# Kernel optimization log

Hardware: AMD Instinct MI355X
Metric: run time of the kernel (lower is better)

## Reference

```python
import jax, jax.numpy as jnp
import numpy as np

IOU_THRESHOLD = 0.3
NUM_CLASSES = 80
BG_IDX = NUM_CLASSES
EPS = 1e-09
TOPK_FALLBACK = 3


def _make_boxes(key, shape, img=640.0):
    # shape = (..., 4); produce valid x1y1x2y2 boxes
    k1, k2 = jax.random.split(key)
    xy = jax.random.uniform(k1, shape[:-1] + (2,)) * img
    wh = jax.random.uniform(k2, shape[:-1] + (2,)) * 128.0 + 8.0
    return jnp.concatenate([xy - wh / 2, xy + wh / 2], axis=-1).astype(jnp.float32)


def setup_inputs() -> dict:
    key = jax.random.key(0)
    ks = jax.random.split(key, 6)
    bs, A, G = 16, 33600, 64
    pd_scores = jax.random.normal(ks[0], (bs, A, NUM_CLASSES), dtype=jnp.float32)
    pd_bboxes = _make_boxes(ks[1], (bs, A, 4))
    anc_points = jax.random.uniform(ks[2], (A, 2), dtype=jnp.float32) * 640.0
    gt_labels = jax.random.randint(ks[3], (bs, G, 1), 0, NUM_CLASSES).astype(jnp.int64)
    gt_bboxes = _make_boxes(ks[4], (bs, G, 4))
    mask_gt = jax.random.randint(ks[5], (bs, G, 1), 0, 2).astype(jnp.int32)
    return {"pd_scores": pd_scores, "pd_bboxes": pd_bboxes, "anc_points": anc_points,
            "gt_labels": gt_labels, "gt_bboxes": gt_bboxes, "mask_gt": mask_gt}


def _pairwise_iou(gt, pd):
    # gt: (bs, G, 4), pd: (bs, A, 4) -> (bs, G, A)
    b1 = gt[:, :, None, :]   # (bs, G, 1, 4)
    b2 = pd[:, None, :, :]   # (bs, 1, A, 4)
    iw = jnp.clip(jnp.minimum(b1[..., 2], b2[..., 2]) - jnp.maximum(b1[..., 0], b2[..., 0]), 0)
    ih = jnp.clip(jnp.minimum(b1[..., 3], b2[..., 3]) - jnp.maximum(b1[..., 1], b2[..., 1]), 0)
    inter = iw * ih
    a1 = (b1[..., 2] - b1[..., 0]) * (b1[..., 3] - b1[..., 1])
    a2 = (b2[..., 2] - b2[..., 0]) * (b2[..., 3] - b2[..., 1])
    return inter / (a1 + a2 - inter + EPS)


def reference(pd_scores, pd_bboxes, anc_points, gt_labels, gt_bboxes, mask_gt):
    bs, G, _ = gt_bboxes.shape
    A = anc_points.shape[0]
    valid = mask_gt[..., 0].astype(bool)                      # (bs, G)

    # IoU matrix; rows of invalid GTs are zero (original writes only valid rows)
    overlaps = _pairwise_iou(gt_bboxes, pd_bboxes) * valid[:, :, None]  # (bs, G, A)

    pos_mask = (overlaps > IOU_THRESHOLD) & valid[:, :, None]
    fg_any = pos_mask.any(axis=(1, 2))                        # (bs,)

    # Per-batch top-k fallback when a batch has zero positives but has valid GTs
    masked = jnp.where(valid[:, :, None], overlaps, -jnp.inf)
    top_vals, _ = jax.lax.top_k(masked.reshape(bs, G * A), TOPK_FALLBACK)
    min_iou = top_vals[:, -1]                                 # (bs,)
    fb_pos = (overlaps >= min_iou[:, None, None]) & valid[:, :, None]
    has_valid = valid.any(axis=1)
    need_fb = (~fg_any) & has_valid
    pos_mask = jnp.where(need_fb[:, None, None], fb_pos, pos_mask)
    fg_mask = pos_mask.any(axis=1)                            # (bs, A)

    # Assignment: argmax over GT axis (first-max, like torch.argmax)
    target_gt_idx = jnp.argmax(overlaps, axis=1)              # (bs, A)

    batch_idx = jnp.arange(bs)[:, None]
    valid_assign = valid[batch_idx, target_gt_idx]            # (bs, A)
    mask = fg_mask & valid_assign

    labels_g = gt_labels[..., 0][batch_idx, target_gt_idx]    # (bs, A)
    target_labels = jnp.where(mask, labels_g, BG_IDX).astype(jnp.int64)
    boxes_g = gt_bboxes[batch_idx, target_gt_idx]             # (bs, A, 4)
    target_bboxes = boxes_g * mask[..., None].astype(boxes_g.dtype)
    # one_hot zeroes out-of-range class indices, matching the explicit range check
    target_scores = jax.nn.one_hot(labels_g, NUM_CLASSES, dtype=jnp.float32) * mask[..., None]

    return (target_labels, target_bboxes, target_scores, fg_mask, target_gt_idx)
```

## Files before the change

### kernel.cpp

```cpp
#include <hip/hip_runtime.h>
#include <math.h>

#define NC 80
constexpr int BS  = 16;
constexpr int NA  = 33600;
constexpr int NG  = 64;
constexpr int TPB = 256;
constexpr int NBLK = (NA + TPB - 1) / TPB;
constexpr int NW   = TPB / 64;
constexpr int NC4  = NC / 4;

typedef float f32x4 __attribute__((ext_vector_type(4)));

__device__ __forceinline__ void ins3(float v, float& t0, float& t1, float& t2) {
  t2 = fmaxf(t2, fminf(v, t1));
  t1 = fmaxf(t1, fminf(v, t0));
  t0 = fmaxf(t0, v);
}

__device__ __forceinline__ void wave_top3(float& t0, float& t1, float& t2) {
  #pragma unroll
  for (int off = 32; off > 0; off >>= 1) {
    float u0 = __shfl_xor(t0, off, 64);
    float u1 = __shfl_xor(t1, off, 64);
    float u2 = __shfl_xor(t2, off, 64);
    ins3(u0, t0, t1, t2);
    ins3(u1, t0, t1, t2);
    ins3(u2, t0, t1, t2);
  }
}

__global__ __launch_bounds__(TPB) void p1_kernel(
    const float4* __restrict__ pd, const float4* __restrict__ gt,
    const int* __restrict__ glab, const int* __restrict__ gmask,
    float* __restrict__ outL, float4* __restrict__ outB,
    float* __restrict__ outS, float* __restrict__ outF,
    float* __restrict__ outI, float* __restrict__ blockTop)
{
  #pragma clang fp contract(off)
  const int b   = blockIdx.y;
  const int tid = threadIdx.x;

  __shared__ float4 sbox[NG];
  __shared__ float  sarea[NG];
  __shared__ int    slab[NG];
  __shared__ int    svalid[NG];
  __shared__ int    scls[TPB];

  const int a0  = blockIdx.x * TPB;
  const int a   = a0 + tid;
  const bool inb = a < NA;

  float4 p = make_float4(0.f, 0.f, 0.f, 0.f);
  if (inb) p = pd[(long)b * NA + a];

  if (tid < NG) {
    int v = gmask[b * NG + tid];
    float4 g = gt[b * NG + tid];
    if (!v) g = make_float4(0.f, 0.f, 0.f, 0.f);
    sbox[tid]   = g;
    sarea[tid]  = (g.z - g.x) * (g.w - g.y);
    slab[tid]   = glab[b * NG + tid];
    svalid[tid] = v;
  }
  __syncthreads();

  float best = -1.f;
  int   bidx = 0;
  float a2 = 0.f;
  bool  maskv = false;
  int   blab  = 0;

  if (inb) {
    a2 = (p.z - p.x) * (p.w - p.y);
    #pragma unroll 8
    for (int g = 0; g < NG; ++g) {
      float4 gb = sbox[g];
      float iw = fminf(gb.z, p.z) - fmaxf(gb.x, p.x);
      float ih = fminf(gb.w, p.w) - fmaxf(gb.y, p.y);
      iw = fmaxf(iw, 0.f);
      ih = fmaxf(ih, 0.f);
      float inter = iw * ih;
      float den   = sarea[g] + a2 - inter + 1e-9f;
      float iou   = inter / den;
      bidx = (iou > best) ? g : bidx;
      best = fmaxf(best, iou);
    }
    bool fg = best > 0.3f;
    maskv = fg && (svalid[bidx] != 0);
    blab  = slab[bidx];
    long ga = (long)b * NA + a;
    outL[ga] = maskv ? (float)blab : 80.f;
    float m = maskv ? 1.f : 0.f;
    float4 gb = sbox[bidx];
    outB[ga] = make_float4(gb.x * m, gb.y * m, gb.z * m, gb.w * m);
    outF[ga] = fg ? 1.f : 0.f;
    outI[ga] = (float)bidx;
  }
  scls[tid] = maskv ? blab : -1;

  float wmax = best;
  #pragma unroll
  for (int off = 32; off > 0; off >>= 1)
    wmax = fmaxf(wmax, __shfl_xor(wmax, off, 64));

  float* bt = blockTop + (((long)b * NBLK + blockIdx.x) * NW + (tid >> 6)) * 3;

  if (wmax <= 0.3f) {
    float t0 = -INFINITY, t1 = -INFINITY, t2 = -INFINITY;
    if (inb) {
      #pragma unroll 4
      for (int g = 0; g < NG; ++g) {
        float4 gb = sbox[g];
        float iw = fminf(gb.z, p.z) - fmaxf(gb.x, p.x);
        float ih = fminf(gb.w, p.w) - fmaxf(gb.y, p.y);
        iw = fmaxf(iw, 0.f);
        ih = fmaxf(ih, 0.f);
        float inter = iw * ih;
        float den   = sarea[g] + a2 - inter + 1e-9f;
        float iou   = inter / den;
        ins3(iou, t0, t1, t2);
      }
    }
    wave_top3(t0, t1, t2);
    if ((tid & 63) == 0) { bt[1] = t1; bt[2] = t2; }
  }
  if ((tid & 63) == 0) bt[0] = wmax;

  __syncthreads();

  const int nA   = min(TPB, NA - a0);
  const int cnt4 = nA * NC4;
  f32x4* s4 = reinterpret_cast<f32x4*>(outS + ((long)b * NA + a0) * NC);
  for (int i = tid; i < cnt4; i += TPB) {
    int row = i / NC4;
    int c0  = (i - row * NC4) * 4;
    int cls = scls[row];
    f32x4 v;
    v.x = (cls == c0    ) ? 1.f : 0.f;
    v.y = (cls == c0 + 1) ? 1.f : 0.f;
    v.z = (cls == c0 + 2) ? 1.f : 0.f;
    v.w = (cls == c0 + 3) ? 1.f : 0.f;
    __builtin_nontemporal_store(v, s4 + i);
  }
}

__global__ __launch_bounds__(TPB) void p3_kernel(
    const float4* __restrict__ pd, const float4* __restrict__ gt,
    const int* __restrict__ glab, const int* __restrict__ gmask,
    const float* __restrict__ blockTop,
    float* __restrict__ outL, float4* __restrict__ outB,
    float* __restrict__ outS, float* __restrict__ outF)
{
  #pragma clang fp contract(off)
  const int b   = blockIdx.y;
  const int tid = threadIdx.x;

  __shared__ float  swm[NW];
  __shared__ float  sM;
  __shared__ float  swt[NW][3];
  __shared__ float  sres;
  __shared__ int    sfb;
  __shared__ float4 sbox[NG];
  __shared__ float  sarea[NG];
  __shared__ int    slab[NG];
  __shared__ int    svalid[NG];

  float m = -INFINITY;
  for (int i = tid; i < NBLK * NW; i += TPB)
    m = fmaxf(m, blockTop[((long)b * NBLK * NW + i) * 3]);
  #pragma unroll
  for (int off = 32; off > 0; off >>= 1)
    m = fmaxf(m, __shfl_xor(m, off, 64));
  const int lane = tid & 63, wid = tid >> 6;
  if (lane == 0) swm[wid] = m;
  __syncthreads();
  if (tid == 0) {
    float r = swm[0];
    #pragma unroll
    for (int w = 1; w < NW; ++w) r = fmaxf(r, swm[w]);
    sM = r;
  }
  __syncthreads();
  if (sM > 0.3f) return;

  int gv = (tid < NG) ? gmask[b * NG + tid] : 0;
  unsigned long long bal = __ballot(gv != 0);

  float t0 = -INFINITY, t1 = -INFINITY, t2 = -INFINITY;
  for (int i = tid; i < NBLK * NW; i += TPB) {
    const float* bt = blockTop + ((long)b * NBLK * NW + i) * 3;
    ins3(bt[0], t0, t1, t2);
    ins3(bt[1], t0, t1, t2);
    ins3(bt[2], t0, t1, t2);
  }
  wave_top3(t0, t1, t2);
  if (lane == 0) { swt[wid][0] = t0; swt[wid][1] = t1; swt[wid][2] = t2; }
  __syncthreads();
  if (tid == 0) {
    float r0 = swt[0][0], r1 = swt[0][1], r2 = swt[0][2];
    #pragma unroll
    for (int w = 1; w < NW; ++w) {
      ins3(swt[w][0], r0, r1, r2);
      ins3(swt[w][1], r0, r1, r2);
      ins3(swt[w][2], r0, r1, r2);
    }
    sfb  = (!(r0 > 0.3f) && bal != 0ULL) ? 1 : 0;
    sres = r2;
  }
  if (tid < NG) {
    float4 g = gt[b * NG + tid];
    if (!gv) g = make_float4(0.f, 0.f, 0.f, 0.f);
    sbox[tid]   = g;
    sarea[tid]  = (g.z - g.x) * (g.w - g.y);
    slab[tid]   = glab[b * NG + tid];
    svalid[tid] = gv;
  }
  __syncthreads();
  if (sfb == 0) return;
  const float minio = sres;

  const int a = blockIdx.x * TPB + tid;
  if (a >= NA) return;

  float4 p  = pd[(long)b * NA + a];
  float  a2 = (p.z - p.x) * (p.w - p.y);
  float best = -1.f;
  int   bidx = 0;
  #pragma unroll 8
  for (int g = 0; g < NG; ++g) {
    float4 gb = sbox[g];
    float iw = fminf(gb.z, p.z) - fmaxf(gb.x, p.x);
    float ih = fminf(gb.w, p.w) - fmaxf(gb.y, p.y);
    iw = fmaxf(iw, 0.f);
    ih = fmaxf(ih, 0.f);
    float inter = iw * ih;
    float den   = sarea[g] + a2 - inter + 1e-9f;
    float iou   = inter / den;
    bidx = (iou > best) ? g : bidx;
    best = fmaxf(best, iou);
  }
  bool fg    = best >= minio;
  bool maskv = fg && (svalid[bidx] != 0);
  int  blab  = slab[bidx];
  long ga = (long)b * NA + a;
  outL[ga] = maskv ? (float)blab : 80.f;
  float mm = maskv ? 1.f : 0.f;
  float4 gb = sbox[bidx];
  outB[ga] = make_float4(gb.x * mm, gb.y * mm, gb.z * mm, gb.w * mm);
  outF[ga] = fg ? 1.f : 0.f;
  if (maskv) outS[ga * NC + blab] = 1.f;
}

extern "C" void kernel_launch(void* const* d_in, const int* in_sizes, int n_in,
                              void* d_out, int out_size, void* d_ws, size_t ws_size,
                              hipStream_t stream) {
  const float4* pd    = (const float4*)d_in[1];
  const int*    glab  = (const int*)d_in[3];
  const float4* gt    = (const float4*)d_in[4];
  const int*    gmask = (const int*)d_in[5];

  float* outf = (float*)d_out;
  float*  outL = outf;
  float4* outB = (float4*)(outf + (long)BS * NA);
  float*  outS = outf + (long)BS * NA * 5;
  float*  outF = outf + (long)BS * NA * 5 + (long)BS * NA * NC;
  float*  outI = outF + (long)BS * NA;

  float* blockTop = (float*)d_ws;

  dim3 grid(NBLK, BS);
  p1_kernel<<<grid, TPB, 0, stream>>>(pd, gt, glab, gmask,
                                      outL, outB, outS, outF, outI, blockTop);
  p3_kernel<<<grid, TPB, 0, stream>>>(pd, gt, glab, gmask, blockTop,
                                      outL, outB, outS, outF);
}
```

Measured before the change: 284.6 us.

## Write one-hot scores per wave via shuffles and shrink fallback grid to one block per batch

In p1, each wave now writes the one-hot score rows for its own 64 anchors, taking class indices from lanes with shuffles instead of a shared array. This removes the block-wide barrier and the shared-memory staging before the large store loop. p3 now launches one block per batch, and that block loops over all anchors. Previously every one of the many blocks re-reduced the whole blockTop array only to exit early. The cost is that the fallback path, when it is taken, runs serially on only 16 blocks, which would be very slow for that case.

Result: no change. 282.2 us (-0.9%).

```diff
diff --git a/kernel.cpp b/kernel.cpp
--- a/kernel.cpp
+++ b/kernel.cpp
@@ -45,7 +45,6 @@
   __shared__ float  sarea[NG];
   __shared__ int    slab[NG];
   __shared__ int    svalid[NG];
-  __shared__ int    scls[TPB];
 
   const int a0  = blockIdx.x * TPB;
   const int a   = a0 + tid;
@@ -97,14 +96,34 @@
     outF[ga] = fg ? 1.f : 0.f;
     outI[ga] = (float)bidx;
   }
-  scls[tid] = maskv ? blab : -1;
+
+  const int lane = tid & 63, wid = tid >> 6;
+  const int nA    = min(TPB, NA - a0);
+  const int wrow0 = wid * 64;
+  const int rows  = min(64, nA - wrow0);
+  const int own_cls = maskv ? blab : -1;
+  if (rows > 0) {
+    f32x4* s4 = reinterpret_cast<f32x4*>(outS + ((long)b * NA + a0 + wrow0) * NC);
+    const int cnt4 = rows * NC4;
+    for (int i = lane; i < cnt4; i += 64) {
+      int row = i / NC4;
+      int c0  = (i - row * NC4) * 4;
+      int cls = __shfl(own_cls, row, 64);
+      f32x4 v;
+      v.x = (cls == c0    ) ? 1.f : 0.f;
+      v.y = (cls == c0 + 1) ? 1.f : 0.f;
+      v.z = (cls == c0 + 2) ? 1.f : 0.f;
+      v.w = (cls == c0 + 3) ? 1.f : 0.f;
+      __builtin_nontemporal_store(v, s4 + i);
+    }
+  }
 
   float wmax = best;
   #pragma unroll
   for (int off = 32; off > 0; off >>= 1)
     wmax = fmaxf(wmax, __shfl_xor(wmax, off, 64));
 
-  float* bt = blockTop + (((long)b * NBLK + blockIdx.x) * NW + (tid >> 6)) * 3;
+  float* bt = blockTop + (((long)b * NBLK + blockIdx.x) * NW + wid) * 3;
 
   if (wmax <= 0.3f) {
     float t0 = -INFINITY, t1 = -INFINITY, t2 = -INFINITY;
@@ -123,26 +142,9 @@
       }
     }
     wave_top3(t0, t1, t2);
-    if ((tid & 63) == 0) { bt[1] = t1; bt[2] = t2; }
-  }
-  if ((tid & 63) == 0) bt[0] = wmax;
-
-  __syncthreads();
-
-  const int nA   = min(TPB, NA - a0);
-  const int cnt4 = nA * NC4;
-  f32x4* s4 = reinterpret_cast<f32x4*>(outS + ((long)b * NA + a0) * NC);
-  for (int i = tid; i < cnt4; i += TPB) {
-    int row = i / NC4;
-    int c0  = (i - row * NC4) * 4;
-    int cls = scls[row];
-    f32x4 v;
-    v.x = (cls == c0    ) ? 1.f : 0.f;
-    v.y = (cls == c0 + 1) ? 1.f : 0.f;
-    v.z = (cls == c0 + 2) ? 1.f : 0.f;
-    v.w = (cls == c0 + 3) ? 1.f : 0.f;
-    __builtin_nontemporal_store(v, s4 + i);
-  }
+    if (lane == 0) { bt[1] = t1; bt[2] = t2; }
+  }
+  if (lane == 0) bt[0] = wmax;
 }
 
 __global__ __launch_bounds__(TPB) void p3_kernel(
@@ -153,7 +155,7 @@
     float* __restrict__ outS, float* __restrict__ outF)
 {
   #pragma clang fp contract(off)
-  const int b   = blockIdx.y;
+  const int b   = blockIdx.x;
   const int tid = threadIdx.x;
 
   __shared__ float  swm[NW];
@@ -220,36 +222,35 @@
   if (sfb == 0) return;
   const float minio = sres;
 
-  const int a = blockIdx.x * TPB + tid;
-  if (a >= NA) return;
-
-  float4 p  = pd[(long)b * NA + a];
-  float  a2 = (p.z - p.x) * (p.w - p.y);
-  float best = -1.f;
-  int   bidx = 0;
-  #pragma unroll 8
-  for (int g = 0; g < NG; ++g) {
-    float4 gb = sbox[g];
-    float iw = fminf(gb.z, p.z) - fmaxf(gb.x, p.x);
-    float ih = fminf(gb.w, p.w) - fmaxf(gb.y, p.y);
-    iw = fmaxf(iw, 0.f);
-    ih = fmaxf(ih, 0.f);
-    float inter = iw * ih;
-    float den   = sarea[g] + a2 - inter + 1e-9f;
-    float iou   = inter / den;
-    bidx = (iou > best) ? g : bidx;
-    best = fmaxf(best, iou);
-  }
-  bool fg    = best >= minio;
-  bool maskv = fg && (svalid[bidx] != 0);
-  int  blab  = slab[bidx];
-  long ga = (long)b * NA + a;
-  outL[ga] = maskv ? (float)blab : 80.f;
-  float mm = maskv ? 1.f : 0.f;
-  float4 gb = sbox[bidx];
-  outB[ga] = make_float4(gb.x * mm, gb.y * mm, gb.z * mm, gb.w * mm);
-  outF[ga] = fg ? 1.f : 0.f;
-  if (maskv) outS[ga * NC + blab] = 1.f;
+  for (int a = tid; a < NA; a += TPB) {
+    float4 p  = pd[(long)b * NA + a];
+    float  a2 = (p.z - p.x) * (p.w - p.y);
+    float best = -1.f;
+    int   bidx = 0;
+    #pragma unroll 8
+    for (int g = 0; g < NG; ++g) {
+      float4 gb = sbox[g];
+      float iw = fminf(gb.z, p.z) - fmaxf(gb.x, p.x);
+      float ih = fminf(gb.w, p.w) - fmaxf(gb.y, p.y);
+      iw = fmaxf(iw, 0.f);
+      ih = fmaxf(ih, 0.f);
+      float inter = iw * ih;
+      float den   = sarea[g] + a2 - inter + 1e-9f;
+      float iou   = inter / den;
+      bidx = (iou > best) ? g : bidx;
+      best = fmaxf(best, iou);
+    }
+    bool fg    = best >= minio;
+    bool maskv = fg && (svalid[bidx] != 0);
+    int  blab  = slab[bidx];
+    long ga = (long)b * NA + a;
+    outL[ga] = maskv ? (float)blab : 80.f;
+    float mm = maskv ? 1.f : 0.f;
+    float4 gb = sbox[bidx];
+    outB[ga] = make_float4(gb.x * mm, gb.y * mm, gb.z * mm, gb.w * mm);
+    outF[ga] = fg ? 1.f : 0.f;
+    if (maskv) outS[ga * NC + blab] = 1.f;
+  }
 }
 
 extern "C" void kernel_launch(void* const* d_in, const int* in_sizes, int n_in,
@@ -272,6 +273,6 @@
   dim3 grid(NBLK, BS);
   p1_kernel<<<grid, TPB, 0, stream>>>(pd, gt, glab, gmask,
                                       outL, outB, outS, outF, outI, blockTop);
-  p3_kernel<<<grid, TPB, 0, stream>>>(pd, gt, glab, gmask, blockTop,
-                                      outL, outB, outS, outF);
-}
+  p3_kernel<<<BS, TPB, 0, stream>>>(pd, gt, glab, gmask, blockTop,
+                                    outL, outB, outS, outF);
+}
```
